# Optimization experiments

Measured on AMD Instinct MI355X. Metric: run time of the kernel, lower is better.

The kernel has to match this reference:

```python
import jax, jax.numpy as jnp
import numpy as np

N_NODES = 50000
N_EDGES = 800000
IN_DIM, HID_DIM, OUT_DIM = 1024, 256, 512


def setup_inputs() -> dict:
    key = jax.random.key(0)
    ks = jax.random.split(key, 8)
    x = jax.random.normal(ks[0], (N_NODES, IN_DIM), dtype=jnp.float32)
    edge_index = jax.random.randint(ks[1], (2, N_EDGES), 0, N_NODES, dtype=jnp.int64)
    # Glorot-ish scaled weights; PyG SAGEConv: out = lin_l(mean_aggr) + lin_r(x), bias in lin_l
    w1_l = jax.random.normal(ks[2], (HID_DIM, IN_DIM), dtype=jnp.float32) / np.sqrt(IN_DIM)
    w1_r = jax.random.normal(ks[3], (HID_DIM, IN_DIM), dtype=jnp.float32) / np.sqrt(IN_DIM)
    b1 = jnp.zeros((HID_DIM,), dtype=jnp.float32)
    w2_l = jax.random.normal(ks[4], (OUT_DIM, HID_DIM), dtype=jnp.float32) / np.sqrt(HID_DIM)
    w2_r = jax.random.normal(ks[5], (OUT_DIM, HID_DIM), dtype=jnp.float32) / np.sqrt(HID_DIM)
    b2 = jnp.zeros((OUT_DIM,), dtype=jnp.float32)
    return {"x": x, "edge_index": edge_index, "w1_l": w1_l, "w1_r": w1_r, "b1": b1,
            "w2_l": w2_l, "w2_r": w2_r, "b2": b2}


def _sage_conv(x, edge_index, w_l, w_r, b):
    """PyG SAGEConv with mean aggregation: lin_l(mean_{j in N(i)} x_j) + lin_r(x_i)."""
    src, dst = edge_index[0], edge_index[1]
    n = x.shape[0]
    # gather source features and scatter-mean into destinations (the memory-bound part)
    agg = jax.ops.segment_sum(x[src], dst, num_segments=n)          # [N, d_in]
    cnt = jax.ops.segment_sum(jnp.ones_like(src, dtype=x.dtype), dst, num_segments=n)
    mean = agg / jnp.maximum(cnt, 1.0)[:, None]                     # empty neighborhoods -> 0
    return mean @ w_l.T + x @ w_r.T + b


def reference(x, edge_index, w1_l, w1_r, b1, w2_l, w2_r, b2):
    # layer 1 + relu (dropout is identity in eval mode)
    h = jax.nn.relu(_sage_conv(x, edge_index, w1_l, w1_r, b1))
    # final layer, no activation
    return _sage_conv(h, edge_index, w2_l, w2_r, b2)
```

## Files before the change

### kernel.cpp

```cpp
#include <hip/hip_runtime.h>


#define IN_DIM  1024
#define HID_DIM 256
#define OUT_N   512

typedef __attribute__((ext_vector_type(8))) short bf16x8;
typedef __attribute__((ext_vector_type(4))) float f32x4;

static __device__ __forceinline__ unsigned short f2bf(float f) {
  unsigned int u = __float_as_uint(f);
  u += 0x7fffu + ((u >> 16) & 1u);
  return (unsigned short)(u >> 16);
}
static __device__ __forceinline__ float bf2f(unsigned short b) {
  return __uint_as_float(((unsigned int)b) << 16);
}

static __device__ __forceinline__ int load_idx(const void* ei, long long pos, int is64) {
  if (is64) return (int)((const long long*)ei)[pos];
  return ((const int*)ei)[pos];
}

__global__ void k_pre(const unsigned int* __restrict__ eiu, const void* __restrict__ ei,
                      int* __restrict__ flag,
                      const float* __restrict__ w1l, const float* __restrict__ w1r,
                      unsigned short* __restrict__ W1c,
                      const float* __restrict__ w2l, const float* __restrict__ w2r,
                      unsigned short* __restrict__ W2c,
                      const float* __restrict__ x, unsigned short* __restrict__ xbf,
                      int n4, int nxb, int nE, int* __restrict__ deg) {
  int b = blockIdx.x;
  if (b == 0) {
    if (threadIdx.x < 64) {
      unsigned int v = eiu[2 * threadIdx.x + 1];
      unsigned long long m = __ballot(v == 0u);
      if (threadIdx.x == 0) *flag = (m == ~0ull) ? 1 : 0;
    }
    return;
  }
  if (b < 513) {
    int i = (b - 1) * 256 + threadIdx.x;
    int base = i * 4;
    int n = base / IN_DIM, k = base % IN_DIM;
    const float* s = (n < HID_DIM) ? &w1l[(size_t)n * IN_DIM + k]
                                   : &w1r[(size_t)(n - HID_DIM) * IN_DIM + k];
    float4 v = *(const float4*)s;
    ushort4 o = { f2bf(v.x), f2bf(v.y), f2bf(v.z), f2bf(v.w) };
    *(ushort4*)&W1c[base] = o;
    return;
  }
  if (b < 769) {
    int i = (b - 513) * 256 + threadIdx.x;
    int base = i * 4;
    int n = base >> 9, k = base & 511;
    const float* s = (k < HID_DIM) ? &w2l[(size_t)n * HID_DIM + k]
                                   : &w2r[(size_t)n * HID_DIM + (k - HID_DIM)];
    float4 v = *(const float4*)s;
    ushort4 o = { f2bf(v.x), f2bf(v.y), f2bf(v.z), f2bf(v.w) };
    *(ushort4*)&W2c[base] = o;
    return;
  }
  if (b < 769 + nxb) {
    int i = (b - 769) * 256 + threadIdx.x;
    if (i >= n4) return;
    float4 v = ((const float4*)x)[i];
    ushort4 o = { f2bf(v.x), f2bf(v.y), f2bf(v.z), f2bf(v.w) };
    ((ushort4*)xbf)[i] = o;
    return;
  }
  __shared__ int s_is64;
  if (threadIdx.x < 64) {
    unsigned int v = eiu[2 * threadIdx.x + 1];
    unsigned long long m = __ballot(v == 0u);
    if (threadIdx.x == 0) s_is64 = (m == ~0ull) ? 1 : 0;
  }
  __syncthreads();
  int e = (b - 769 - nxb) * 256 + threadIdx.x;
  if (e < nE) {
    int d = load_idx(ei, (long long)nE + e, s_is64);
    atomicAdd(&deg[d], 1);
  }
}

__global__ void k_bsum(const int* __restrict__ deg, int* __restrict__ bsum) {
  int t = threadIdx.x;
  int4 d4 = ((const int4*)(deg + (size_t)blockIdx.x * 1024))[t];
  int v = d4.x + d4.y + d4.z + d4.w;
#pragma unroll
  for (int d = 1; d < 64; d <<= 1) v += __shfl_xor(v, d);
  __shared__ int ws[4];
  if ((t & 63) == 0) ws[t >> 6] = v;
  __syncthreads();
  if (t == 0) bsum[blockIdx.x] = ws[0] + ws[1] + ws[2] + ws[3];
}

__global__ __launch_bounds__(1024) void k_bscan(int* __restrict__ bsum, int nb) {
  __shared__ int s[1024];
  int t = threadIdx.x;
  s[t] = (t < nb) ? bsum[t] : 0;
  __syncthreads();
  for (int d = 1; d < 1024; d <<= 1) {
    int v = (t >= d) ? s[t - d] : 0;
    __syncthreads();
    s[t] += v;
    __syncthreads();
  }
  if (t < nb) bsum[t] = s[t];
}

__global__ __launch_bounds__(256) void k_offsets(const int* __restrict__ deg,
                                                 const int* __restrict__ bsumInc,
                                                 int* __restrict__ off,
                                                 int* __restrict__ cursor) {
  const int t = threadIdx.x;
  const int l = t & 63, w = t >> 6;
  const size_t base = (size_t)blockIdx.x * 1024;
  int4 d4 = ((const int4*)(deg + base))[t];
  int tsum = d4.x + d4.y + d4.z + d4.w;
  int incl = tsum;
#pragma unroll
  for (int d = 1; d < 64; d <<= 1) {
    int u = __shfl_up(incl, d);
    if (l >= d) incl += u;
  }
  __shared__ int wt[4];
  if (l == 63) wt[w] = incl;
  __syncthreads();
  int wpre = 0;
  for (int i = 0; i < w; ++i) wpre += wt[i];
  int bpre = (blockIdx.x == 0) ? 0 : bsumInc[blockIdx.x - 1];
  int excl = bpre + wpre + incl - tsum;
  int4 o;
  o.x = excl;
  o.y = excl + d4.x;
  o.z = o.y + d4.y;
  o.w = o.z + d4.z;
  ((int4*)(off + base))[t] = o;
  ((int4*)(cursor + base))[t] = o;
}

static __device__ __forceinline__ void load_lds16(const void* g, void* lds) {
  __builtin_amdgcn_global_load_lds(
      (const __attribute__((address_space(1))) unsigned int*)g,
      (__attribute__((address_space(3))) unsigned int*)lds, 16, 0, 0);
}

static __device__ __forceinline__ int xcd_swz(int orig, int nwg) {
  const int q = nwg >> 3, r = nwg & 7;
  const int xcd = orig & 7, rk = orig >> 3;
  return (xcd < r) ? xcd * (q + 1) + rk : r * (q + 1) + (xcd - r) * q + rk;
}

__global__ __launch_bounds__(256) void k_g1f(const unsigned short* __restrict__ A,
                                             const unsigned short* __restrict__ B,
                                             unsigned short* __restrict__ Cl,
                                             unsigned short* __restrict__ Cr,
                                             const float* __restrict__ b1,
                                             int ngemm,
                                             const void* __restrict__ ei, int nE,
                                             const int* __restrict__ flag,
                                             int* __restrict__ cursor,
                                             int* __restrict__ csr) {
  if ((int)blockIdx.x >= ngemm) {
    int e = ((int)blockIdx.x - ngemm) * 256 + threadIdx.x;
    if (e < nE) {
      int is64 = *flag;
      int s = load_idx(ei, e, is64);
      int d = load_idx(ei, (long long)nE + e, is64);
      int p = atomicAdd(&cursor[d], 1);
      csr[p] = s;
    }
    return;
  }
  __shared__ unsigned short As[2][128 * 32];
  __shared__ unsigned short Bs[2][128 * 32];
  const int tid = threadIdx.x;
  const int w = tid >> 6, l = tid & 63;
  const int wm = w >> 1, wn = w & 1;
  const int quad = l >> 4, lane16 = l & 15;
  const int wg = xcd_swz(blockIdx.x, ngemm);
  const int m0 = (wg >> 2) * 128;
  const int n0 = (wg & 3) * 128;

  const int flat0 = ((w * 2 + 0) << 10), flat1 = ((w * 2 + 1) << 10);
  const int row0 = (flat0 + l * 16) >> 6, cb0 = (flat0 + l * 16) & 63;
  const int row1 = (flat1 + l * 16) >> 6, cb1 = (flat1 + l * 16) & 63;
  const unsigned short* Ar0 = A + (size_t)(m0 + row0) * IN_DIM + (cb0 >> 1);
  const unsigned short* Ar1 = A + (size_t)(m0 + row1) * IN_DIM + (cb1 >> 1);
  const unsigned short* Br0 = B + (size_t)(n0 + row0) * IN_DIM + (cb0 >> 1);
  const unsigned short* Br1 = B + (size_t)(n0 + row1) * IN_DIM + (cb1 >> 1);

  auto STAGE = [&](int k0, int buf) {
    load_lds16(Ar0 + k0, (char*)As[buf] + flat0);
    load_lds16(Br0 + k0, (char*)Bs[buf] + flat0);
    load_lds16(Ar1 + k0, (char*)As[buf] + flat1);
    load_lds16(Br1 + k0, (char*)Bs[buf] + flat1);
  };

  f32x4 acc[4][4] = {};
  STAGE(0, 0);
  __syncthreads();
  int cur = 0;
  for (int k0 = 0; k0 < IN_DIM; k0 += 32) {
    if (k0 + 32 < IN_DIM) STAGE(k0 + 32, cur ^ 1);
    bf16x8 af[4], bfr[4];
#pragma unroll
    for (int i = 0; i < 4; ++i)
      af[i] = *(const bf16x8*)&As[cur][(wm * 64 + i * 16 + lane16) * 32 + quad * 8];
#pragma unroll
    for (int j = 0; j < 4; ++j)
      bfr[j] = *(const bf16x8*)&Bs[cur][(wn * 64 + j * 16 + lane16) * 32 + quad * 8];
#pragma unroll
    for (int i = 0; i < 4; ++i)
#pragma unroll
      for (int j = 0; j < 4; ++j)
        acc[i][j] = __builtin_amdgcn_mfma_f32_16x16x32_bf16(af[i], bfr[j], acc[i][j], 0, 0, 0);
    __syncthreads();
    cur ^= 1;
  }

  const bool right = (n0 >= 256);
  unsigned short* Cb = right ? Cr : Cl;
  const int nc0 = n0 - (right ? 256 : 0);
#pragma unroll
  for (int i = 0; i < 4; ++i) {
    const int rbase = m0 + wm * 64 + i * 16 + quad * 4;
#pragma unroll
    for (int j = 0; j < 4; ++j) {
      const int col = nc0 + wn * 64 + j * 16 + lane16;
      const float bv = right ? b1[col] : 0.0f;
#pragma unroll
      for (int r = 0; r < 4; ++r)
        Cb[(size_t)(rbase + r) * HID_DIM + col] = f2bf(acc[i][j][r] + bv);
    }
  }
}

__global__ __launch_bounds__(256) void k_gemm2(const unsigned short* __restrict__ Am,
                                               const unsigned short* __restrict__ Ah,
                                               const unsigned short* __restrict__ B,
                                               float* __restrict__ out,
                                               const float* __restrict__ b2, int Mstore) {
  __shared__ unsigned short As[2][128 * 32];
  __shared__ unsigned short Bs[2][128 * 32];
  const int tid = threadIdx.x;
  const int w = tid >> 6, l = tid & 63;
  const int wm = w >> 1, wn = w & 1;
  const int quad = l >> 4, lane16 = l & 15;
  const int nwg = gridDim.x * gridDim.y;
  const int wg = xcd_swz(blockIdx.y * gridDim.x + blockIdx.x, nwg);
  const int m0 = (wg / gridDim.x) * 128;
  const int n0 = (wg % gridDim.x) * 128;

  const int flat0 = ((w * 2 + 0) << 10), flat1 = ((w * 2 + 1) << 10);
  const int row0 = (flat0 + l * 16) >> 6, cb0 = (flat0 + l * 16) & 63;
  const int row1 = (flat1 + l * 16) >> 6, cb1 = (flat1 + l * 16) & 63;

  auto STAGE = [&](int kk, int buf) {
    const unsigned short* Abase = (kk < HID_DIM) ? Am + kk : Ah + (kk - HID_DIM);
    load_lds16(Abase + (size_t)(m0 + row0) * HID_DIM + (cb0 >> 1), (char*)As[buf] + flat0);
    load_lds16(B + (size_t)(n0 + row0) * (2 * HID_DIM) + (kk + (cb0 >> 1)), (char*)Bs[buf] + flat0);
    load_lds16(Abase + (size_t)(m0 + row1) * HID_DIM + (cb1 >> 1), (char*)As[buf] + flat1);
    load_lds16(B + (size_t)(n0 + row1) * (2 * HID_DIM) + (kk + (cb1 >> 1)), (char*)Bs[buf] + flat1);
  };

  f32x4 acc[4][4] = {};
  STAGE(0, 0);
  __syncthreads();
  int cur = 0;
  for (int k0 = 0; k0 < 2 * HID_DIM; k0 += 32) {
    if (k0 + 32 < 2 * HID_DIM) STAGE(k0 + 32, cur ^ 1);
    bf16x8 af[4], bfr[4];
#pragma unroll
    for (int i = 0; i < 4; ++i)
      af[i] = *(const bf16x8*)&As[cur][(wm * 64 + i * 16 + lane16) * 32 + quad * 8];
#pragma unroll
    for (int j = 0; j < 4; ++j)
      bfr[j] = *(const bf16x8*)&Bs[cur][(wn * 64 + j * 16 + lane16) * 32 + quad * 8];
#pragma unroll
    for (int i = 0; i < 4; ++i)
#pragma unroll
      for (int j = 0; j < 4; ++j)
        acc[i][j] = __builtin_amdgcn_mfma_f32_16x16x32_bf16(af[i], bfr[j], acc[i][j], 0, 0, 0);
    __syncthreads();
    cur ^= 1;
  }

#pragma unroll
  for (int i = 0; i < 4; ++i) {
    const int rbase = m0 + wm * 64 + i * 16 + quad * 4;
#pragma unroll
    for (int j = 0; j < 4; ++j) {
      const int col = n0 + wn * 64 + j * 16 + lane16;
      const float bv = b2[col];
#pragma unroll
      for (int r = 0; r < 4; ++r) {
        const int rowi = rbase + r;
        if (rowi < Mstore) out[(size_t)rowi * OUT_N + col] = acc[i][j][r] + bv;
      }
    }
  }
}

template <int NB>
static __device__ __forceinline__ void gatherN(const unsigned short* __restrict__ src,
                                               const int* __restrict__ csr, int ib,
                                               size_t colb, float* a) {
  bf16x8 v[NB];
#pragma unroll
  for (int u = 0; u < NB; ++u) {
    int r = csr[ib + 2 * u];
    v[u] = *(const bf16x8*)&src[(size_t)r * HID_DIM + colb];
  }
#pragma unroll
  for (int u = 0; u < NB; ++u)
#pragma unroll
    for (int c = 0; c < 8; ++c) a[c] += bf2f((unsigned short)v[u][c]);
}

static __device__ __forceinline__ void agg_sum(const unsigned short* __restrict__ src,
                                               const int* __restrict__ csr,
                                               int s, int e, int half, size_t colb,
                                               float* a) {
  const int cnt = e - s;
  const int P = cnt >> 1;
  const int ib0 = s + half;
  int k = 0;
  for (; k + 8 <= P; k += 8) gatherN<8>(src, csr, ib0 + 2 * k, colb, a);
  if (k + 4 <= P) { gatherN<4>(src, csr, ib0 + 2 * k, colb, a); k += 4; }
  if (k + 2 <= P) { gatherN<2>(src, csr, ib0 + 2 * k, colb, a); k += 2; }
  if (k < P)      { gatherN<1>(src, csr, ib0 + 2 * k, colb, a); }
  if ((cnt & 1) && half == 0) {
    bf16x8 v = *(const bf16x8*)&src[(size_t)csr[e - 1] * HID_DIM + colb];
#pragma unroll
    for (int c = 0; c < 8; ++c) a[c] += bf2f((unsigned short)v[c]);
  }
#pragma unroll
  for (int c = 0; c < 8; ++c) a[c] += __shfl_xor(a[c], 32);
}

__global__ void k_agg1(const unsigned short* __restrict__ Cl,
                       const unsigned short* __restrict__ Cr,
                       const int* __restrict__ off, const int* __restrict__ csr,
                       unsigned short* __restrict__ h, int nNodes) {
  int node = blockIdx.x * 4 + (threadIdx.x >> 6);
  if (node >= nNodes) return;
  const int l = threadIdx.x & 63;
  const int half = l >> 5, li = l & 31;
  const size_t colb = (size_t)li * 8;
  int s = off[node], e = off[node + 1];
  float a[8] = {};
  agg_sum(Cl, csr, s, e, half, colb, a);
  if (half == 0) {
    float inv = 1.0f / fmaxf((float)(e - s), 1.0f);
    bf16x8 xr = *(const bf16x8*)&Cr[(size_t)node * HID_DIM + colb];
    bf16x8 o;
#pragma unroll
    for (int c = 0; c < 8; ++c)
      o[c] = (short)f2bf(fmaxf(a[c] * inv + bf2f((unsigned short)xr[c]), 0.0f));
    *(bf16x8*)&h[(size_t)node * HID_DIM + colb] = o;
  }
}

__global__ void k_agg2(const unsigned short* __restrict__ hsrc,
                       const int* __restrict__ off, const int* __restrict__ csr,
                       unsigned short* __restrict__ mean2, int nNodes) {
  int node = blockIdx.x * 4 + (threadIdx.x >> 6);
  if (node >= nNodes) return;
  const int l = threadIdx.x & 63;
  const int half = l >> 5, li = l & 31;
  const size_t colb = (size_t)li * 8;
  int s = off[node], e = off[node + 1];
  float a[8] = {};
  agg_sum(hsrc, csr, s, e, half, colb, a);
  if (half == 0) {
    float inv = 1.0f / fmaxf((float)(e - s), 1.0f);
    bf16x8 o;
#pragma unroll
    for (int c = 0; c < 8; ++c) o[c] = (short)f2bf(a[c] * inv);
    *(bf16x8*)&mean2[(size_t)node * HID_DIM + colb] = o;
  }
}

extern "C" void kernel_launch(void* const* d_in, const int* in_sizes, int n_in,
                              void* d_out, int out_size, void* d_ws, size_t ws_size,
                              hipStream_t stream) {
  const float* x   = (const float*)d_in[0];
  const void*  ei  = d_in[1];
  const float* w1l = (const float*)d_in[2];
  const float* w1r = (const float*)d_in[3];
  const float* b1  = (const float*)d_in[4];
  const float* w2l = (const float*)d_in[5];
  const float* w2r = (const float*)d_in[6];
  const float* b2  = (const float*)d_in[7];
  float* out = (float*)d_out;

  const int nN   = in_sizes[0] / IN_DIM;
  const int nE   = in_sizes[1] / 2;
  const int Mpad = (nN + 127) & ~127;
  const int padN = (nN + 1023) & ~1023;
  const int nb   = padN >> 10;

  char* ws = (char*)d_ws;
  size_t o = 0;
  auto alloc = [&](size_t bytes) {
    char* p = ws + o;
    o += (bytes + 255) & ~(size_t)255;
    return p;
  };
  unsigned short* xbf   = (unsigned short*)alloc((size_t)Mpad * IN_DIM * 2);
  unsigned short* W1c   = (unsigned short*)alloc((size_t)2 * HID_DIM * IN_DIM * 2);
  unsigned short* W2c   = (unsigned short*)alloc((size_t)OUT_N * 2 * HID_DIM * 2);
  unsigned short* Cl    = (unsigned short*)alloc((size_t)Mpad * HID_DIM * 2);
  unsigned short* Cr    = (unsigned short*)alloc((size_t)Mpad * HID_DIM * 2);
  unsigned short* hbuf  = (unsigned short*)alloc((size_t)Mpad * HID_DIM * 2);
  unsigned short* mean2 = (unsigned short*)alloc((size_t)Mpad * HID_DIM * 2);
  int* deg    = (int*)alloc((size_t)padN * 4);
  int* offs   = (int*)alloc((size_t)padN * 4);
  int* cursor = (int*)alloc((size_t)padN * 4);
  int* bsum   = (int*)alloc((size_t)1024 * 4);
  int* csr    = (int*)alloc((size_t)nE * 4);
  int* flag   = (int*)alloc(256);

  hipMemsetAsync(deg, 0, (size_t)padN * 4, stream);

  const int n4  = nN * IN_DIM / 4;
  const int nxb = (n4 + 255) / 256;
  const int nEb = (nE + 255) / 256;
  const int ngemm = 4 * (Mpad / 128);

  k_pre<<<769 + nxb + nEb, 256, 0, stream>>>((const unsigned int*)ei, ei, flag,
                                             w1l, w1r, W1c, w2l, w2r, W2c,
                                             x, xbf, n4, nxb, nE, deg);
  k_bsum<<<nb, 256, 0, stream>>>(deg, bsum);
  k_bscan<<<1, 1024, 0, stream>>>(bsum, nb);
  k_offsets<<<nb, 256, 0, stream>>>(deg, bsum, offs, cursor);
  k_g1f<<<ngemm + nEb, 256, 0, stream>>>(xbf, W1c, Cl, Cr, b1, ngemm,
                                         ei, nE, flag, cursor, csr);
  k_agg1<<<(nN + 3) / 4, 256, 0, stream>>>(Cl, Cr, offs, csr, hbuf, nN);
  k_agg2<<<(nN + 3) / 4, 256, 0, stream>>>(hbuf, offs, csr, mean2, nN);
  dim3 g2(512 / 128, Mpad / 128);
  k_gemm2<<<g2, 256, 0, stream>>>(mean2, hbuf, W2c, out, b2, nN);
}
```

Measured before the change: 675.2 us.

## Use XOR-swizzled single-buffer BK=64 LDS tiles in both GEMM kernels

```diff
diff --git a/kernel.cpp b/kernel.cpp
--- a/kernel.cpp
+++ b/kernel.cpp
@@ -173,8 +173,8 @@
     }
     return;
   }
-  __shared__ unsigned short As[2][128 * 32];
-  __shared__ unsigned short Bs[2][128 * 32];
+  __shared__ unsigned short As[128 * 64];
+  __shared__ unsigned short Bs[128 * 64];
   const int tid = threadIdx.x;
   const int w = tid >> 6, l = tid & 63;
   const int wm = w >> 1, wn = w & 1;
@@ -183,41 +183,54 @@
   const int m0 = (wg >> 2) * 128;
   const int n0 = (wg & 3) * 128;
 
-  const int flat0 = ((w * 2 + 0) << 10), flat1 = ((w * 2 + 1) << 10);
-  const int row0 = (flat0 + l * 16) >> 6, cb0 = (flat0 + l * 16) & 63;
-  const int row1 = (flat1 + l * 16) >> 6, cb1 = (flat1 + l * 16) & 63;
-  const unsigned short* Ar0 = A + (size_t)(m0 + row0) * IN_DIM + (cb0 >> 1);
-  const unsigned short* Ar1 = A + (size_t)(m0 + row1) * IN_DIM + (cb1 >> 1);
-  const unsigned short* Br0 = B + (size_t)(n0 + row0) * IN_DIM + (cb0 >> 1);
-  const unsigned short* Br1 = B + (size_t)(n0 + row1) * IN_DIM + (cb1 >> 1);
-
-  auto STAGE = [&](int k0, int buf) {
-    load_lds16(Ar0 + k0, (char*)As[buf] + flat0);
-    load_lds16(Br0 + k0, (char*)Bs[buf] + flat0);
-    load_lds16(Ar1 + k0, (char*)As[buf] + flat1);
-    load_lds16(Br1 + k0, (char*)Bs[buf] + flat1);
-  };
+  const unsigned short* asrc[4];
+  const unsigned short* bsrc[4];
+#pragma unroll
+  for (int it = 0; it < 4; ++it) {
+    const int p_lin = (w * 4 + it) * 64 + l;
+    const int row = p_lin >> 3;
+    const int c = (p_lin & 7) ^ (row & 7);
+    asrc[it] = A + (size_t)(m0 + row) * IN_DIM + c * 8;
+    bsrc[it] = B + (size_t)(n0 + row) * IN_DIM + c * 8;
+  }
+  int arb[4], brb[4];
+#pragma unroll
+  for (int i = 0; i < 4; ++i) {
+    arb[i] = wm * 64 + i * 16 + lane16;
+    brb[i] = wn * 64 + i * 16 + lane16;
+  }
 
   f32x4 acc[4][4] = {};
-  STAGE(0, 0);
-  __syncthreads();
-  int cur = 0;
-  for (int k0 = 0; k0 < IN_DIM; k0 += 32) {
-    if (k0 + 32 < IN_DIM) STAGE(k0 + 32, cur ^ 1);
-    bf16x8 af[4], bfr[4];
-#pragma unroll
-    for (int i = 0; i < 4; ++i)
-      af[i] = *(const bf16x8*)&As[cur][(wm * 64 + i * 16 + lane16) * 32 + quad * 8];
-#pragma unroll
-    for (int j = 0; j < 4; ++j)
-      bfr[j] = *(const bf16x8*)&Bs[cur][(wn * 64 + j * 16 + lane16) * 32 + quad * 8];
-#pragma unroll
-    for (int i = 0; i < 4; ++i)
-#pragma unroll
-      for (int j = 0; j < 4; ++j)
-        acc[i][j] = __builtin_amdgcn_mfma_f32_16x16x32_bf16(af[i], bfr[j], acc[i][j], 0, 0, 0);
-    __syncthreads();
-    cur ^= 1;
+  for (int k0 = 0; k0 < IN_DIM; k0 += 64) {
+#pragma unroll
+    for (int it = 0; it < 4; ++it)
+      load_lds16(asrc[it] + k0, (char*)As + ((w * 4 + it) << 10));
+#pragma unroll
+    for (int it = 0; it < 4; ++it)
+      load_lds16(bsrc[it] + k0, (char*)Bs + ((w * 4 + it) << 10));
+    __syncthreads();
+#pragma unroll
+    for (int kk = 0; kk < 2; ++kk) {
+      bf16x8 af[4], bfr[4];
+#pragma unroll
+      for (int i = 0; i < 4; ++i) {
+        const int r = arb[i];
+        af[i] = *(const bf16x8*)((const char*)As + r * 128 +
+                                 (((kk * 4 + quad) ^ (r & 7)) << 4));
+      }
+#pragma unroll
+      for (int j = 0; j < 4; ++j) {
+        const int r = brb[j];
+        bfr[j] = *(const bf16x8*)((const char*)Bs + r * 128 +
+                                  (((kk * 4 + quad) ^ (r & 7)) << 4));
+      }
+#pragma unroll
+      for (int i = 0; i < 4; ++i)
+#pragma unroll
+        for (int j = 0; j < 4; ++j)
+          acc[i][j] = __builtin_amdgcn_mfma_f32_16x16x32_bf16(af[i], bfr[j], acc[i][j], 0, 0, 0);
+    }
+    __syncthreads();
   }
 
   const bool right = (n0 >= 256);
@@ -242,8 +255,8 @@
                                                const unsigned short* __restrict__ B,
                                                float* __restrict__ out,
                                                const float* __restrict__ b2, int Mstore) {
-  __shared__ unsigned short As[2][128 * 32];
-  __shared__ unsigned short Bs[2][128 * 32];
+  __shared__ unsigned short As[128 * 64];
+  __shared__ unsigned short Bs[128 * 64];
   const int tid = threadIdx.x;
   const int w = tid >> 6, l = tid & 63;
   const int wm = w >> 1, wn = w & 1;
@@ -253,38 +266,56 @@
   const int m0 = (wg / gridDim.x) * 128;
   const int n0 = (wg % gridDim.x) * 128;
 
-  const int flat0 = ((w * 2 + 0) << 10), flat1 = ((w * 2 + 1) << 10);
-  const int row0 = (flat0 + l * 16) >> 6, cb0 = (flat0 + l * 16) & 63;
-  const int row1 = (flat1 + l * 16) >> 6, cb1 = (flat1 + l * 16) & 63;
-
-  auto STAGE = [&](int kk, int buf) {
-    const unsigned short* Abase = (kk < HID_DIM) ? Am + kk : Ah + (kk - HID_DIM);
-    load_lds16(Abase + (size_t)(m0 + row0) * HID_DIM + (cb0 >> 1), (char*)As[buf] + flat0);
-    load_lds16(B + (size_t)(n0 + row0) * (2 * HID_DIM) + (kk + (cb0 >> 1)), (char*)Bs[buf] + flat0);
-    load_lds16(Abase + (size_t)(m0 + row1) * HID_DIM + (cb1 >> 1), (char*)As[buf] + flat1);
-    load_lds16(B + (size_t)(n0 + row1) * (2 * HID_DIM) + (kk + (cb1 >> 1)), (char*)Bs[buf] + flat1);
-  };
+  int arow[4], acol[4];
+  const unsigned short* bsrc[4];
+#pragma unroll
+  for (int it = 0; it < 4; ++it) {
+    const int p_lin = (w * 4 + it) * 64 + l;
+    const int row = p_lin >> 3;
+    const int c = (p_lin & 7) ^ (row & 7);
+    arow[it] = row; acol[it] = c * 8;
+    bsrc[it] = B + (size_t)(n0 + row) * (2 * HID_DIM) + c * 8;
+  }
+  int arb[4], brb[4];
+#pragma unroll
+  for (int i = 0; i < 4; ++i) {
+    arb[i] = wm * 64 + i * 16 + lane16;
+    brb[i] = wn * 64 + i * 16 + lane16;
+  }
 
   f32x4 acc[4][4] = {};
-  STAGE(0, 0);
-  __syncthreads();
-  int cur = 0;
-  for (int k0 = 0; k0 < 2 * HID_DIM; k0 += 32) {
-    if (k0 + 32 < 2 * HID_DIM) STAGE(k0 + 32, cur ^ 1);
-    bf16x8 af[4], bfr[4];
-#pragma unroll
-    for (int i = 0; i < 4; ++i)
-      af[i] = *(const bf16x8*)&As[cur][(wm * 64 + i * 16 + lane16) * 32 + quad * 8];
-#pragma unroll
-    for (int j = 0; j < 4; ++j)
-      bfr[j] = *(const bf16x8*)&Bs[cur][(wn * 64 + j * 16 + lane16) * 32 + quad * 8];
-#pragma unroll
-    for (int i = 0; i < 4; ++i)
-#pragma unroll
-      for (int j = 0; j < 4; ++j)
-        acc[i][j] = __builtin_amdgcn_mfma_f32_16x16x32_bf16(af[i], bfr[j], acc[i][j], 0, 0, 0);
-    __syncthreads();
-    cur ^= 1;
+  for (int k0 = 0; k0 < 2 * HID_DIM; k0 += 64) {
+    const unsigned short* Ab = (k0 < HID_DIM) ? Am + k0 : Ah + (k0 - HID_DIM);
+#pragma unroll
+    for (int it = 0; it < 4; ++it)
+      load_lds16(Ab + (size_t)(m0 + arow[it]) * HID_DIM + acol[it],
+                 (char*)As + ((w * 4 + it) << 10));
+#pragma unroll
+    for (int it = 0; it < 4; ++it)
+      load_lds16(bsrc[it] + k0, (char*)Bs + ((w * 4 + it) << 10));
+    __syncthreads();
+#pragma unroll
+    for (int kk = 0; kk < 2; ++kk) {
+      bf16x8 af[4], bfr[4];
+#pragma unroll
+      for (int i = 0; i < 4; ++i) {
+        const int r = arb[i];
+        af[i] = *(const bf16x8*)((const char*)As + r * 128 +
+                                 (((kk * 4 + quad) ^ (r & 7)) << 4));
+      }
+#pragma unroll
+      for (int j = 0; j < 4; ++j) {
+        const int r = brb[j];
+        bfr[j] = *(const bf16x8*)((const char*)Bs + r * 128 +
+                                  (((kk * 4 + quad) ^ (r & 7)) << 4));
+      }
+#pragma unroll
+      for (int i = 0; i < 4; ++i)
+#pragma unroll
+        for (int j = 0; j < 4; ++j)
+          acc[i][j] = __builtin_amdgcn_mfma_f32_16x16x32_bf16(af[i], bfr[j], acc[i][j], 0, 0, 0);
+    }
+    __syncthreads();
   }
 
 #pragma unroll
```

New measurement: 647.3 us. -4.1%, faster.
